# Kernel tuning notes

Hardware: AMD Instinct MI355X
Metric: run time of the kernel (lower is better)

## Reference

```python
import jax, jax.numpy as jnp
import numpy as np


def setup_inputs() -> dict:
    key = jax.random.key(0)
    ks = jax.random.split(key, 8)
    B, K, L, D = 8, 8, 4096, 256
    S = 1024  # windowlen
    inp = {
        "input": jax.random.normal(ks[0], (B, K, L, D), dtype=jnp.float32),
        "event_time": jax.random.uniform(ks[1], (B, L), dtype=jnp.float32),
        "W1": jax.random.normal(ks[2], (D, 2 * D), dtype=jnp.float32) / np.sqrt(D),
        "b1": jnp.zeros((2 * D,), dtype=jnp.float32),
        "W2": jax.random.normal(ks[3], (2 * D, D), dtype=jnp.float32) / np.sqrt(2 * D),
        "b2": jnp.zeros((D,), dtype=jnp.float32),
        "W3": jax.random.normal(ks[4], (D, 1), dtype=jnp.float32) / np.sqrt(D),
        "windowlen": S,
    }
    return inp


def reference(input, event_time, W1, b1, W2, b2, W3, windowlen):
    B, K, L, D = input.shape
    S = windowlen
    idx = jnp.arange(0, 2 * S, 2)  # strided window indices, [S]
    x = input.reshape(B * K, L, D)  # (BK, L, D)
    x_s = x[:, idx, :]  # (BK, S, D) indexed gather

    # offset MLP: D -> 2D -> D -> 1 (dropout inactive at eval)
    h = jax.nn.relu(jnp.einsum('bsd,de->bse', x_s, W1) + b1)
    h = jax.nn.relu(jnp.einsum('bse,ed->bsd', h, W2) + b2)
    offset = jnp.einsum('bsd,do->bso', h, W3)  # (BK, S, 1)

    pos = idx.astype(input.dtype)[None, :, None] + offset  # (BK, S, 1)

    # mask: pos <= argmax(event_time) per batch
    limit = jax.lax.stop_gradient(jnp.argmax(event_time, axis=-1)).astype(input.dtype)  # (B,)
    mask = (pos.reshape(B, K, S) <= limit[:, None, None]).astype(jnp.float32)  # (B, K, S)

    # grid x = pos/(L-1)*2-1 un-normalizes back to exactly pos; y=0 hits row 0.
    p = pos[..., 0]  # (BK, S)
    x0 = jnp.floor(p)
    w = p - x0  # fractional weight (grad flows to p, floor is constant)
    i0 = x0.astype(jnp.int32)
    i1 = i0 + 1

    def gather(i):
        valid = ((i >= 0) & (i <= L - 1)).astype(x.dtype)[..., None]
        ic = jnp.clip(i, 0, L - 1)
        return jnp.take_along_axis(x, ic[..., None], axis=1) * valid  # (BK, S, D)

    out = (1.0 - w)[..., None] * gather(i0) + w[..., None] * gather(i1)
    out = out.reshape(B, K, S, D)
    return out, mask
```

## Files before the change

kernel.cpp:

```cpp
#include <hip/hip_runtime.h>
#include <math.h>

#define B_   8
#define K_   8
#define L_   4096
#define D_   256
#define H_   512
#define S_   1024
#define M_   65536
#define MAXF 4096

typedef _Float16 half8  __attribute__((ext_vector_type(8)));
typedef float    floatx4 __attribute__((ext_vector_type(4)));

#define WS_LIMIT   0
#define WS_COUNTER 64
#define WS_FLAGS   128
#define WS_W1F     65536
#define WS_W2F     (65536 + H_*D_*2)

#define XA_LD    264
#define H1_LD    520
#define KS1      8
#define KS2      16

__global__ __launch_bounds__(256) void prep_kernel(const float* __restrict__ et,
                                                   const float* __restrict__ W1,
                                                   const float* __restrict__ W2,
                                                   char* __restrict__ ws) {
  __shared__ float sv[256];
  __shared__ int   si[256];
  const int blk = blockIdx.x;
  const int t   = threadIdx.x;
  if (blk < 1024) {
    int e = blk * 256 + t;
    if (e < H_ * D_) {
      int tile = e >> 9, r = e & 511;
      int l = r >> 3, j = r & 7;
      int ntile = tile >> 3, ks = tile & 7;
      int n = (ntile << 4) + (l & 15);
      int k = (ks << 5) + ((l >> 4) << 3) + j;
      ((_Float16*)(ws + WS_W1F))[e] = (_Float16)W1[(size_t)k * H_ + n];
    } else {
      int e2 = e - H_ * D_;
      int tile = e2 >> 9, r = e2 & 511;
      int l = r >> 3, j = r & 7;
      int ntile = tile >> 4, ks = tile & 15;
      int n = (ntile << 4) + (l & 15);
      int k = (ks << 5) + ((l >> 4) << 3) + j;
      ((_Float16*)(ws + WS_W2F))[e2] = (_Float16)W2[(size_t)k * D_ + n];
    }
  } else if (blk < 1032) {
    int b = blk - 1024;
    const float* row = et + (size_t)b * L_;
    float best = -INFINITY; int bidx = 0;
    for (int i = t; i < L_; i += 256) {
      float v = row[i];
      if (v > best) { best = v; bidx = i; }
    }
    sv[t] = best; si[t] = bidx;
    __syncthreads();
    for (int sft = 128; sft > 0; sft >>= 1) {
      if (t < sft) {
        float v2 = sv[t + sft]; int i2 = si[t + sft];
        if (v2 > sv[t] || (v2 == sv[t] && i2 < si[t])) { sv[t] = v2; si[t] = i2; }
      }
      __syncthreads();
    }
    if (t == 0) ((float*)(ws + WS_LIMIT))[b] = (float)si[0];
  } else {
    if (t == 0) *(int*)(ws + WS_COUNTER) = 0;
  }
}

template<int KS>
__device__ __forceinline__ void gemm_l2b(
    const _Float16* __restrict__ Wf,
    const _Float16* __restrict__ Alds, const int lda,
    const int lane, floatx4 (&acc)[2][4])
{
  const int lr = lane & 15, quad = lane >> 4;
  const _Float16* wl = Wf + lane * 8;
  uint4 Bw[4][4];
  #pragma unroll
  for (int i = 0; i < 4; ++i)
    #pragma unroll
    for (int nt = 0; nt < 4; ++nt)
      Bw[i][nt] = *(const uint4*)(wl + ((size_t)nt * KS + i) * 512);
  #pragma unroll
  for (int ks = 0; ks < KS; ++ks) {
    half8 af0 = *(const half8*)(Alds + lr * lda + ks * 32 + quad * 8);
    half8 af1 = *(const half8*)(Alds + (16 + lr) * lda + ks * 32 + quad * 8);
    #pragma unroll
    for (int nt = 0; nt < 4; ++nt) {
      half8 bfv = *(const half8*)&Bw[ks & 3][nt];
      acc[0][nt] = __builtin_amdgcn_mfma_f32_16x16x32_f16(af0, bfv, acc[0][nt], 0, 0, 0);
      acc[1][nt] = __builtin_amdgcn_mfma_f32_16x16x32_f16(af1, bfv, acc[1][nt], 0, 0, 0);
    }
    if (ks + 4 < KS) {
      #pragma unroll
      for (int nt = 0; nt < 4; ++nt)
        Bw[ks & 3][nt] = *(const uint4*)(wl + ((size_t)nt * KS + ks + 4) * 512);
    }
  }
}

__global__ __launch_bounds__(256) void fused_kernel(
    const float* __restrict__ X, char* __restrict__ ws,
    const float* __restrict__ b1, const float* __restrict__ b2,
    const float* __restrict__ W3,
    float* __restrict__ out, float* __restrict__ maskv) {
  __shared__ __align__(16) _Float16 Xa[32 * XA_LD];
  __shared__ __align__(16) _Float16 h1s[32 * H1_LD];
  __shared__ float psum[4][32];
  __shared__ float posl[32];

  const _Float16* W1f    = (const _Float16*)(ws + WS_W1F);
  const _Float16* W2f    = (const _Float16*)(ws + WS_W2F);
  const float*    limitf = (const float*)(ws + WS_LIMIT);
  int*            counter = (int*)(ws + WS_COUNTER);
  int*            flags   = (int*)(ws + WS_FLAGS);

  const int t    = threadIdx.x;
  const int m0   = blockIdx.x * 32;
  const int lane = t & 63, w = t >> 6;
  const int lr   = lane & 15, quad = lane >> 4;
  const int bk   = m0 >> 10;

  {
    const int r = t >> 3, q = t & 7;
    const int s = (m0 + r) & 1023;
    const float* xrow = X + ((size_t)bk * L_ + 2 * s) * D_ + q * 32;
    _Float16* dst = Xa + r * XA_LD + q * 32;
    #pragma unroll
    for (int i = 0; i < 4; ++i) {
      float4 v0 = *(const float4*)(xrow + i * 8);
      float4 v1 = *(const float4*)(xrow + i * 8 + 4);
      half8 h;
      h[0]=(_Float16)v0.x; h[1]=(_Float16)v0.y; h[2]=(_Float16)v0.z; h[3]=(_Float16)v0.w;
      h[4]=(_Float16)v1.x; h[5]=(_Float16)v1.y; h[6]=(_Float16)v1.z; h[7]=(_Float16)v1.w;
      *(half8*)(dst + i * 8) = h;
    }
  }
  __syncthreads();

  floatx4 acc[2][4];

  #pragma unroll
  for (int nh = 0; nh < 2; ++nh) {
    #pragma unroll
    for (int mt = 0; mt < 2; ++mt)
      #pragma unroll
      for (int nt = 0; nt < 4; ++nt)
        acc[mt][nt] = (floatx4){0.f, 0.f, 0.f, 0.f};
    gemm_l2b<KS1>(W1f + (size_t)(nh * 16 + w * 4) * KS1 * 512, Xa, XA_LD, lane, acc);
    #pragma unroll
    for (int nt = 0; nt < 4; ++nt) {
      int col = nh * 256 + w * 64 + nt * 16 + lr;
      float bias = b1[col];
      #pragma unroll
      for (int mt = 0; mt < 2; ++mt) {
        int rowb = mt * 16 + quad * 4;
        #pragma unroll
        for (int rg = 0; rg < 4; ++rg) {
          float v = acc[mt][nt][rg] + bias;
          h1s[(rowb + rg) * H1_LD + col] = (_Float16)(v > 0.f ? v : 0.f);
        }
      }
    }
  }
  __syncthreads();

  #pragma unroll
  for (int mt = 0; mt < 2; ++mt)
    #pragma unroll
    for (int nt = 0; nt < 4; ++nt)
      acc[mt][nt] = (floatx4){0.f, 0.f, 0.f, 0.f};
  gemm_l2b<KS2>(W2f + (size_t)(w * 4) * KS2 * 512, h1s, H1_LD, lane, acc);

  float part[2][4] = {{0,0,0,0},{0,0,0,0}};
  #pragma unroll
  for (int nt = 0; nt < 4; ++nt) {
    int col = w * 64 + nt * 16 + lr;
    float bias = b2[col];
    float w3   = W3[col];
    #pragma unroll
    for (int mt = 0; mt < 2; ++mt)
      #pragma unroll
      for (int rg = 0; rg < 4; ++rg) {
        float h2 = acc[mt][nt][rg] + bias;
        h2 = h2 > 0.f ? h2 : 0.f;
        part[mt][rg] = fmaf(h2, w3, part[mt][rg]);
      }
  }
  #pragma unroll
  for (int mt = 0; mt < 2; ++mt)
    #pragma unroll
    for (int rg = 0; rg < 4; ++rg) {
      float p = part[mt][rg];
      p += __shfl_xor(p, 1, 64);
      p += __shfl_xor(p, 2, 64);
      p += __shfl_xor(p, 4, 64);
      p += __shfl_xor(p, 8, 64);
      if (lr == 0) psum[w][mt * 16 + quad * 4 + rg] = p;
    }
  __syncthreads();
  if (t < 32) {
    int   mrow  = m0 + t;
    float off   = psum[0][t] + psum[1][t] + psum[2][t] + psum[3][t];
    int   s     = mrow & 1023;
    float pos   = (float)(2 * s) + off;
    float limit = limitf[mrow >> 13];
    maskv[mrow] = (pos <= limit) ? 1.f : 0.f;
    posl[t] = pos;
    float d = pos - limit;
    if (d < 0.5f && d > -0.5f) {
      int idx = atomicAdd(counter, 1);
      if (idx < MAXF) flags[idx] = mrow;
    }
  }
  __syncthreads();
  {
    const int c4 = t & 63, rgp = t >> 6;
    const float* xbase = X + (size_t)bk * (L_ * D_);
    #pragma unroll 4
    for (int rr = 0; rr < 8; ++rr) {
      int   rI = rgp * 8 + rr;
      float p  = posl[rI];
      float x0f = floorf(p);
      float ww  = p - x0f;
      int i0 = (int)x0f, i1 = i0 + 1;
      float v0 = (i0 >= 0 && i0 < L_) ? (1.f - ww) : 0.f;
      float v1 = (i1 >= 0 && i1 < L_) ? ww : 0.f;
      int ic0 = min(max(i0, 0), L_ - 1), ic1 = min(max(i1, 0), L_ - 1);
      float4 g0 = *(const float4*)(xbase + (size_t)ic0 * D_ + c4 * 4);
      float4 g1 = *(const float4*)(xbase + (size_t)ic1 * D_ + c4 * 4);
      float4 o;
      o.x = v0 * g0.x + v1 * g1.x;
      o.y = v0 * g0.y + v1 * g1.y;
      o.z = v0 * g0.z + v1 * g1.z;
      o.w = v0 * g0.w + v1 * g1.w;
      *(float4*)(out + (size_t)(m0 + rI) * D_ + c4 * 4) = o;
    }
  }
}

__global__ __launch_bounds__(256) void fixup_kernel(
    const float* __restrict__ X,  const float* __restrict__ W1,
    const float* __restrict__ b1, const float* __restrict__ W2,
    const float* __restrict__ b2, const float* __restrict__ W3,
    const char* __restrict__ ws, float* __restrict__ maskv) {
  __shared__ float xs[256];
  __shared__ float h1f[512];
  __shared__ float red[4];
  const float* limitf  = (const float*)(ws + WS_LIMIT);
  const int*   counter = (const int*)(ws + WS_COUNTER);
  const int*   flags   = (const int*)(ws + WS_FLAGS);
  const int t = threadIdx.x;
  const int cnt = min(*counter, MAXF);
  for (int fi = blockIdx.x; fi < cnt; fi += 64) {
    int mrow = flags[fi];
    int bk = mrow >> 10, s = mrow & 1023;
    const float* xrow = X + ((size_t)bk * L_ + 2 * s) * D_;
    xs[t] = xrow[t];
    __syncthreads();
    #pragma unroll
    for (int jj = 0; jj < 2; ++jj) {
      int j = t + jj * 256;
      float a = b1[j];
      for (int d = 0; d < 256; ++d)
        a = fmaf(xs[d], W1[(size_t)d * H_ + j], a);
      h1f[j] = a > 0.f ? a : 0.f;
    }
    __syncthreads();
    {
      float a = b2[t];
      for (int e = 0; e < 512; ++e)
        a = fmaf(h1f[e], W2[(size_t)e * D_ + t], a);
      float h2 = a > 0.f ? a : 0.f;
      float pp = h2 * W3[t];
      #pragma unroll
      for (int o = 32; o >= 1; o >>= 1) pp += __shfl_xor(pp, o, 64);
      if ((t & 63) == 0) red[t >> 6] = pp;
    }
    __syncthreads();
    if (t == 0) {
      float off   = red[0] + red[1] + red[2] + red[3];
      float pos   = (float)(2 * s) + off;
      float limit = limitf[mrow >> 13];
      maskv[mrow] = (pos <= limit) ? 1.f : 0.f;
    }
    __syncthreads();
  }
}

extern "C" void kernel_launch(void* const* d_in, const int* in_sizes, int n_in,
                              void* d_out, int out_size, void* d_ws, size_t ws_size,
                              hipStream_t stream) {
  const float* X  = (const float*)d_in[0];
  const float* et = (const float*)d_in[1];
  const float* W1 = (const float*)d_in[2];
  const float* b1 = (const float*)d_in[3];
  const float* W2 = (const float*)d_in[4];
  const float* b2 = (const float*)d_in[5];
  const float* W3 = (const float*)d_in[6];
  float* out   = (float*)d_out;
  float* maskv = out + (size_t)M_ * D_;
  char*  ws    = (char*)d_ws;

  prep_kernel <<<1033, 256, 0, stream>>>(et, W1, W2, ws);
  fused_kernel<<<2048, 256, 0, stream>>>(X, ws, b1, b2, W3, out, maskv);
  fixup_kernel<<<64,   256, 0, stream>>>(X, W1, b1, W2, b2, W3, ws, maskv);
}
```

Measured before the change: 460.1 us.

## Alias LDS buffers, shrink weight prefetch, and remap blocks to raise occupancy

Xa and h1s now share one LDS buffer, made safe by running both layer-1 GEMM halves into separate accumulators before a barrier and then writing h1. This reduces shared memory per block, and together with launch_bounds(256,4) and a weight prefetch depth cut from 4 to 2 k-steps it is meant to allow more resident blocks per CU. The change also adds s_setprio around the MFMA bursts and remaps block IDs so consecutive blocks spread across bk groups. The cost is more live accumulator registers, possible spills under the tighter bound, and less latency hiding for weight loads.

```diff
diff --git a/kernel.cpp b/kernel.cpp
--- a/kernel.cpp
+++ b/kernel.cpp
@@ -81,9 +81,9 @@
 {
   const int lr = lane & 15, quad = lane >> 4;
   const _Float16* wl = Wf + lane * 8;
-  uint4 Bw[4][4];
-  #pragma unroll
-  for (int i = 0; i < 4; ++i)
+  uint4 Bw[2][4];
+  #pragma unroll
+  for (int i = 0; i < 2; ++i)
     #pragma unroll
     for (int nt = 0; nt < 4; ++nt)
       Bw[i][nt] = *(const uint4*)(wl + ((size_t)nt * KS + i) * 512);
@@ -91,29 +91,32 @@
   for (int ks = 0; ks < KS; ++ks) {
     half8 af0 = *(const half8*)(Alds + lr * lda + ks * 32 + quad * 8);
     half8 af1 = *(const half8*)(Alds + (16 + lr) * lda + ks * 32 + quad * 8);
+    __builtin_amdgcn_s_setprio(1);
     #pragma unroll
     for (int nt = 0; nt < 4; ++nt) {
-      half8 bfv = *(const half8*)&Bw[ks & 3][nt];
+      half8 bfv = *(const half8*)&Bw[ks & 1][nt];
       acc[0][nt] = __builtin_amdgcn_mfma_f32_16x16x32_f16(af0, bfv, acc[0][nt], 0, 0, 0);
       acc[1][nt] = __builtin_amdgcn_mfma_f32_16x16x32_f16(af1, bfv, acc[1][nt], 0, 0, 0);
     }
-    if (ks + 4 < KS) {
+    __builtin_amdgcn_s_setprio(0);
+    if (ks + 2 < KS) {
       #pragma unroll
       for (int nt = 0; nt < 4; ++nt)
-        Bw[ks & 3][nt] = *(const uint4*)(wl + ((size_t)nt * KS + ks + 4) * 512);
-    }
-  }
-}
-
-__global__ __launch_bounds__(256) void fused_kernel(
+        Bw[ks & 1][nt] = *(const uint4*)(wl + ((size_t)nt * KS + ks + 2) * 512);
+    }
+  }
+}
+
+__global__ __launch_bounds__(256, 4) void fused_kernel(
     const float* __restrict__ X, char* __restrict__ ws,
     const float* __restrict__ b1, const float* __restrict__ b2,
     const float* __restrict__ W3,
     float* __restrict__ out, float* __restrict__ maskv) {
-  __shared__ __align__(16) _Float16 Xa[32 * XA_LD];
-  __shared__ __align__(16) _Float16 h1s[32 * H1_LD];
+  __shared__ __align__(16) _Float16 u[32 * H1_LD];
   __shared__ float psum[4][32];
   __shared__ float posl[32];
+  _Float16* Xa  = u;
+  _Float16* h1s = u;
 
   const _Float16* W1f    = (const _Float16*)(ws + WS_W1F);
   const _Float16* W2f    = (const _Float16*)(ws + WS_W2F);
@@ -122,7 +125,9 @@
   int*            flags   = (int*)(ws + WS_FLAGS);
 
   const int t    = threadIdx.x;
-  const int m0   = blockIdx.x * 32;
+  const int bid  = blockIdx.x;
+  const int lt   = (bid & 7) * 256 + (bid >> 3);
+  const int m0   = lt * 32;
   const int lane = t & 63, w = t >> 6;
   const int lr   = lane & 15, quad = lane >> 4;
   const int bk   = m0 >> 10;
@@ -144,30 +149,37 @@
   }
   __syncthreads();
 
-  floatx4 acc[2][4];
-
-  #pragma unroll
-  for (int nh = 0; nh < 2; ++nh) {
-    #pragma unroll
-    for (int mt = 0; mt < 2; ++mt)
+  floatx4 accA[2][4], accB[2][4];
+  #pragma unroll
+  for (int mt = 0; mt < 2; ++mt)
+    #pragma unroll
+    for (int nt = 0; nt < 4; ++nt) {
+      accA[mt][nt] = (floatx4){0.f, 0.f, 0.f, 0.f};
+      accB[mt][nt] = (floatx4){0.f, 0.f, 0.f, 0.f};
+    }
+  gemm_l2b<KS1>(W1f + (size_t)(w * 4) * KS1 * 512,        Xa, XA_LD, lane, accA);
+  gemm_l2b<KS1>(W1f + (size_t)(16 + w * 4) * KS1 * 512,   Xa, XA_LD, lane, accB);
+  __syncthreads();
+
+  {
+    auto epi = [&](floatx4 (&a)[2][4], int nh) {
       #pragma unroll
-      for (int nt = 0; nt < 4; ++nt)
-        acc[mt][nt] = (floatx4){0.f, 0.f, 0.f, 0.f};
-    gemm_l2b<KS1>(W1f + (size_t)(nh * 16 + w * 4) * KS1 * 512, Xa, XA_LD, lane, acc);
-    #pragma unroll
-    for (int nt = 0; nt < 4; ++nt) {
-      int col = nh * 256 + w * 64 + nt * 16 + lr;
-      float bias = b1[col];
-      #pragma unroll
-      for (int mt = 0; mt < 2; ++mt) {
-        int rowb = mt * 16 + quad * 4;
+      for (int nt = 0; nt < 4; ++nt) {
+        int col = nh * 256 + w * 64 + nt * 16 + lr;
+        float bias = b1[col];
         #pragma unroll
-        for (int rg = 0; rg < 4; ++rg) {
-          float v = acc[mt][nt][rg] + bias;
-          h1s[(rowb + rg) * H1_LD + col] = (_Float16)(v > 0.f ? v : 0.f);
+        for (int mt = 0; mt < 2; ++mt) {
+          int rowb = mt * 16 + quad * 4;
+          #pragma unroll
+          for (int rg = 0; rg < 4; ++rg) {
+            float v = a[mt][nt][rg] + bias;
+            h1s[(rowb + rg) * H1_LD + col] = (_Float16)(v > 0.f ? v : 0.f);
+          }
         }
       }
-    }
+    };
+    epi(accA, 0);
+    epi(accB, 1);
   }
   __syncthreads();
 
@@ -175,8 +187,8 @@
   for (int mt = 0; mt < 2; ++mt)
     #pragma unroll
     for (int nt = 0; nt < 4; ++nt)
-      acc[mt][nt] = (floatx4){0.f, 0.f, 0.f, 0.f};
-  gemm_l2b<KS2>(W2f + (size_t)(w * 4) * KS2 * 512, h1s, H1_LD, lane, acc);
+      accA[mt][nt] = (floatx4){0.f, 0.f, 0.f, 0.f};
+  gemm_l2b<KS2>(W2f + (size_t)(w * 4) * KS2 * 512, h1s, H1_LD, lane, accA);
 
   float part[2][4] = {{0,0,0,0},{0,0,0,0}};
   #pragma unroll
@@ -188,7 +200,7 @@
     for (int mt = 0; mt < 2; ++mt)
       #pragma unroll
       for (int rg = 0; rg < 4; ++rg) {
-        float h2 = acc[mt][nt][rg] + bias;
+        float h2 = accA[mt][nt][rg] + bias;
         h2 = h2 > 0.f ? h2 : 0.f;
         part[mt][rg] = fmaf(h2, w3, part[mt][rg]);
       }
```

Result: faster. 434.2 us (-5.6%).
